# Kernel optimization log

Hardware: AMD Instinct MI355X
Metric: run time of the kernel (lower is better)

The kernel has to match this reference:

```python
import jax, jax.numpy as jnp
import numpy as np

HIDDEN_DIM = 1024
NUM_EXPERTS = 8
BASE_LR = 0.5
LR_DECAY = 0.85
TOLERANCE = 0.001


def setup_inputs() -> dict:
    key = jax.random.key(0)
    ks = jax.random.split(key, 8)
    B, T, D, E = 4, 2048, HIDDEN_DIM, NUM_EXPERTS
    x_real = jax.random.normal(ks[0], (B, T, D), dtype=jnp.float32)
    x_imag = jax.random.normal(ks[1], (B, T, D), dtype=jnp.float32)
    phase_offset = jax.random.uniform(ks[2], (D,), dtype=jnp.float32) * 2.0 * np.pi
    Wg = jax.random.normal(ks[3], (D, E), dtype=jnp.float32) / np.sqrt(D)
    bg = jnp.zeros((E,), dtype=jnp.float32)
    We = jax.random.normal(ks[4], (E, D, D), dtype=jnp.float32) / np.sqrt(D)
    be = jnp.zeros((E, D), dtype=jnp.float32)
    return {"x_real": x_real, "x_imag": x_imag, "phase_offset": phase_offset,
            "Wg": Wg, "bg": bg, "We": We, "be": be, "local_iterations": 8}


def _moe(z, Wg, bg, We, be, capacity):
    # z: [N, D] complex64. Expert-choice routing on the real part.
    N, D = z.shape
    logits = z.real @ Wg + bg                     # [N, E]
    S = jax.nn.softmax(logits, axis=-1)           # [N, E]
    scores, idx = jax.lax.top_k(S.T, capacity)    # each [E, k]
    gathered = z[idx]                             # [E, k, D] complex
    out_e = jnp.einsum('ekd,edh->ekh', gathered, We.astype(z.dtype)) + be[:, None, :]
    y = jnp.zeros((N, D), z.dtype).at[idx.reshape(-1)].add(
        (scores[..., None] * out_e).reshape(-1, D))
    return y


def _build_target(z, phase_offset):
    # z: [B, T, D] complex; target[t] = z[t-1] * exp(i*phase), target[0] = z[0]
    rot = jnp.exp(1j * phase_offset)              # [D] complex64
    return jnp.concatenate([z[:, :1, :], z[:, :-1, :] * rot], axis=1)


def reference(x_real, x_imag, phase_offset, Wg, bg, We, be, local_iterations):
    B, T, D = x_real.shape
    N = B * T
    capacity = N // NUM_EXPERTS
    z0 = (x_real + 1j * x_imag).astype(jnp.complex64)  # [B, T, D]
    target = _build_target(z0, phase_offset)
    max_iters = max(1, int(local_iterations) - 1)

    def cond(carry):
        it, z, lr, done = carry
        return jnp.logical_and(it < max_iters, jnp.logical_not(done))

    def body(carry):
        it, z, lr, _ = carry
        pred = _moe(z.reshape(N, D), Wg, bg, We, be, capacity).reshape(B, T, D)
        residual = target - pred
        z = z + lr.astype(z.dtype) * residual
        res_mean = jnp.mean(jnp.abs(residual))
        return (it + 1, z, lr * LR_DECAY, res_mean < TOLERANCE)

    it0 = jnp.array(0, jnp.int32)
    lr0 = jnp.array(BASE_LR, jnp.float32)
    iters_run, z_final, _, _ = jax.lax.while_loop(cond, body, (it0, z0, lr0, jnp.array(False)))

    target_grad = _build_target(z0, phase_offset)
    pred_grad = _moe(z_final.reshape(N, D), Wg, bg, We, be, capacity).reshape(B, T, D)
    out = z_final + BASE_LR * (target_grad - pred_grad)   # [B, T, D] complex
    out_stacked = jnp.stack([out.real, out.imag], axis=-1)  # [B, T, D, 2] float32
    return out_stacked, iters_run
```

## Files before the change

kernel.cpp:

```cpp
#include <hip/hip_runtime.h>
#include <math.h>

#define ND    8388608
#define NTOK  8192
#define DIM   1024
#define NEXP  8
#define CAP   1024
#define TSEQ  2048

typedef short bf16x8 __attribute__((ext_vector_type(8)));
typedef unsigned short u16x8 __attribute__((ext_vector_type(8)));
typedef float f32x4 __attribute__((ext_vector_type(4)));

#define AS1 __attribute__((address_space(1)))
#define AS3 __attribute__((address_space(3)))

__device__ __forceinline__ void gload_lds16(const void* g, void* l) {
    __builtin_amdgcn_global_load_lds((const AS1 unsigned int*)g,
                                     (AS3 unsigned int*)l, 16, 0, 0);
}

__device__ __forceinline__ unsigned short f2bf(float x) {
    union { float f; unsigned u; } v; v.f = x;
    unsigned r = v.u + 0x7FFFu + ((v.u >> 16) & 1u);
    return (unsigned short)(r >> 16);
}
__device__ __forceinline__ float bf2f(unsigned short b) {
    union { unsigned u; float f; } v; v.u = ((unsigned)b) << 16; return v.f;
}

__global__ void k_init_small(const float* __restrict__ phase, const int* __restrict__ Lptr,
                             float* __restrict__ rc, float* __restrict__ rs,
                             int* __restrict__ ctl) {
    int d = blockIdx.x * blockDim.x + threadIdx.x;
    if (d < DIM) { rc[d] = cosf(phase[d]); rs[d] = sinf(phase[d]); }
    if (d == 0) {
        ctl[0] = 0; ctl[1] = 0;
        int L = Lptr[0]; int mi = L - 1; if (mi < 1) mi = 1;
        ctl[2] = mi;
    }
}

__global__ void k_init_big(const float* __restrict__ xr, const float* __restrict__ xi,
                           float* __restrict__ zre, unsigned short* __restrict__ zimB) {
    int i = blockIdx.x * blockDim.x + threadIdx.x;
    if (i >= ND) return;
    zre[i] = xr[i];
    zimB[i] = f2bf(xi[i]);
}

__global__ __launch_bounds__(256) void k_wconv(const float* __restrict__ We,
                                               unsigned short* __restrict__ Whi,
                                               unsigned short* __restrict__ Wlo) {
    __shared__ float lds[64][65];
    int e = blockIdx.z, h0 = blockIdx.x * 64, d0 = blockIdx.y * 64;
    int tid = threadIdx.x;
    #pragma unroll
    for (int q = 0; q < 16; ++q) {
        int idx = q * 256 + tid;
        int i = idx >> 6, j = idx & 63;
        lds[i][j] = We[(size_t)e * 1048576 + (size_t)(d0 + i) * 1024 + h0 + j];
    }
    __syncthreads();
    #pragma unroll
    for (int q = 0; q < 2; ++q) {
        int sid = q * 256 + tid;
        int j = sid >> 3, sp = sid & 7;
        int h = h0 + j;
        int slog = sp ^ (h & 7);
        u16x8 hi, lo;
        #pragma unroll
        for (int u = 0; u < 8; ++u) {
            float x = lds[slog * 8 + u][j];
            unsigned short hb = f2bf(x);
            hi[u] = hb;
            lo[u] = f2bf(x - bf2f(hb));
        }
        size_t o = (((size_t)(e << 10) + h) << 10) + d0 + sp * 8;
        *(u16x8*)(Whi + o) = hi;
        *(u16x8*)(Wlo + o) = lo;
    }
}

__global__ __launch_bounds__(256) void k_gate(
    const float* __restrict__ zre, const float* __restrict__ Wg, const float* __restrict__ bg,
    float* __restrict__ S, int* __restrict__ tokcnt,
    const int* __restrict__ ctl, int iter) {
    if (iter >= 0 && (ctl[0] || iter >= ctl[2])) return;
    const int w = threadIdx.x >> 6, lane = threadIdx.x & 63;
    const int n = blockIdx.x * 4 + w;
    const float* zr = zre + ((size_t)n << 10);
    float acc[8] = {0,0,0,0,0,0,0,0};
    #pragma unroll
    for (int q = 0; q < 4; ++q) {
        const int d0 = q * 256 + lane * 4;
        float4 zv = *(const float4*)(zr + d0);
        float zz[4] = {zv.x, zv.y, zv.z, zv.w};
        #pragma unroll
        for (int j = 0; j < 4; ++j) {
            const float4 w0 = *(const float4*)(Wg + (d0 + j) * 8);
            const float4 w1 = *(const float4*)(Wg + (d0 + j) * 8 + 4);
            acc[0] += zz[j] * w0.x; acc[1] += zz[j] * w0.y; acc[2] += zz[j] * w0.z; acc[3] += zz[j] * w0.w;
            acc[4] += zz[j] * w1.x; acc[5] += zz[j] * w1.y; acc[6] += zz[j] * w1.z; acc[7] += zz[j] * w1.w;
        }
    }
    #pragma unroll
    for (int off = 32; off > 0; off >>= 1)
        #pragma unroll
        for (int e = 0; e < 8; ++e) acc[e] += __shfl_xor(acc[e], off);
    if (lane == 0) {
        float m = -1e30f;
        #pragma unroll
        for (int e = 0; e < 8; ++e) { acc[e] += bg[e]; m = fmaxf(m, acc[e]); }
        float sum = 0.f;
        #pragma unroll
        for (int e = 0; e < 8; ++e) { acc[e] = expf(acc[e] - m); sum += acc[e]; }
        float inv = 1.0f / sum;
        *(float4*)(S + (n << 3))     = (float4){acc[0]*inv, acc[1]*inv, acc[2]*inv, acc[3]*inv};
        *(float4*)(S + (n << 3) + 4) = (float4){acc[4]*inv, acc[5]*inv, acc[6]*inv, acc[7]*inv};
        tokcnt[n] = 0;
    }
}

__global__ __launch_bounds__(1024) void k_route(
    const float* __restrict__ S, int* __restrict__ idxs, int* __restrict__ tokcnt,
    int* __restrict__ ent_id, const int* __restrict__ ctl, int iter) {
    if (iter >= 0 && (ctl[0] || iter >= ctl[2])) return;
    __shared__ unsigned keys[NTOK];
    __shared__ unsigned hA[2048];
    __shared__ unsigned hB[2048];
    __shared__ int sbkt, srem, sntie, scnt;
    const int e = blockIdx.x, tid = threadIdx.x;
    if (tid == 0) scnt = 0;
    for (int n = tid; n < NTOK; n += 1024) keys[n] = __float_as_uint(S[(n << 3) + e]);
    __syncthreads();

    int rem = CAP;
    unsigned pref = 0;
    #pragma unroll
    for (int lvl = 0; lvl < 3; ++lvl) {
        const int nb = (lvl == 2) ? 1024 : 2048;
        for (int i = tid; i < nb; i += 1024) hA[i] = 0;
        __syncthreads();
        for (int n = tid; n < NTOK; n += 1024) {
            unsigned k = keys[n];
            bool ok; unsigned b;
            if (lvl == 0)      { ok = true;                 b = k >> 21; }
            else if (lvl == 1) { ok = (k >> 21) == pref;    b = (k >> 10) & 2047u; }
            else               { ok = (k >> 10) == pref;    b = k & 1023u; }
            if (ok) atomicAdd(&hA[b], 1u);
        }
        __syncthreads();
        unsigned* src = hA; unsigned* dst = hB;
        for (int off = 1; off < nb; off <<= 1) {
            for (int i = tid; i < nb; i += 1024)
                dst[i] = src[i] + ((i + off < nb) ? src[i + off] : 0u);
            __syncthreads();
            unsigned* t = src; src = dst; dst = t;
        }
        for (int i = tid; i < nb; i += 1024) {
            unsigned sfi = src[i];
            unsigned sfn = (i + 1 < nb) ? src[i + 1] : 0u;
            if (sfi >= (unsigned)rem && sfn < (unsigned)rem) {
                sbkt = i; srem = rem - (int)sfn; sntie = (int)(sfi - sfn);
            }
        }
        __syncthreads();
        int b = sbkt; rem = srem;
        if (lvl == 0)      pref = (unsigned)b;
        else if (lvl == 1) pref = (pref << 11) | (unsigned)b;
        else               pref = (pref << 10) | (unsigned)b;
        __syncthreads();
    }
    const unsigned T = pref;
    const int remv = rem;
    const bool allt = (remv == sntie);

    for (int n = tid; n < NTOK; n += 1024) {
        unsigned k = keys[n];
        bool sel = (k > T);
        if (k == T) {
            if (allt) sel = true;
            else {
                int r = 0;
                int j = 0;
                for (; j + 8 <= n; j += 8) {
                    r += (int)(keys[j] == T) + (int)(keys[j+1] == T) + (int)(keys[j+2] == T)
                       + (int)(keys[j+3] == T) + (int)(keys[j+4] == T) + (int)(keys[j+5] == T)
                       + (int)(keys[j+6] == T) + (int)(keys[j+7] == T);
                }
                for (; j < n; ++j) r += (int)(keys[j] == T);
                sel = (r < remv);
            }
        }
        if (sel) {
            int slot = atomicAdd(&scnt, 1);
            int row = (e << 10) + slot;
            idxs[row] = n;
            int p = atomicAdd(&tokcnt[n], 1);
            ent_id[(n << 3) + p] = row;
        }
    }
}

__global__ __launch_bounds__(256) void k_gather_convert(
    const float* __restrict__ zre, const int* __restrict__ idxs,
    unsigned short* __restrict__ Ahi, unsigned short* __restrict__ Alo,
    const int* __restrict__ ctl, int iter) {
    if (iter >= 0 && (ctl[0] || iter >= ctl[2])) return;
    int g = blockIdx.x * 256 + threadIdx.x;
    int r = g >> 7;
    int sl = g & 127;
    int c = sl >> 3, sp = sl & 7;
    int slog = sp ^ (r & 7);
    int n = idxs[r];
    const float* src = zre + ((size_t)n << 10) + c * 64 + slog * 8;
    u16x8 hi, lo;
    #pragma unroll
    for (int u = 0; u < 8; ++u) {
        float x = src[u];
        unsigned short hb = f2bf(x);
        hi[u] = hb;
        lo[u] = f2bf(x - bf2f(hb));
    }
    size_t o = ((size_t)r << 10) + c * 64 + sp * 8;
    *(u16x8*)(Ahi + o) = hi;
    *(u16x8*)(Alo + o) = lo;
}

__global__ __launch_bounds__(256, 2) void k_gemm_cx(
    const unsigned short* __restrict__ Ahi, const unsigned short* __restrict__ Alo,
    const unsigned short* __restrict__ zimB,
    const unsigned short* __restrict__ Whi, const unsigned short* __restrict__ Wlo,
    const float* __restrict__ be, const int* __restrict__ idxs,
    float* __restrict__ outre, float* __restrict__ outim,
    const int* __restrict__ ctl, int iter) {
    if (iter >= 0 && (ctl[0] || iter >= ctl[2])) return;
    extern __shared__ unsigned short smem[];
    const int bid = blockIdx.x;
    const int e = bid & 7, bx = (bid >> 3) & 7, by = bid >> 6;
    const int tid = threadIdx.x;
    const int wid = tid >> 6, lane = tid & 63;
    const int wm = wid >> 1, wn = wid & 1;

    const unsigned short* srcbase;
    int rowbase, tofs;
    if (wid == 0)      { srcbase = Ahi; rowbase = (e << 10) + by * 128; tofs = 0; }
    else if (wid == 1) { srcbase = Alo; rowbase = (e << 10) + by * 128; tofs = 8192; }
    else if (wid == 2) { srcbase = Whi; rowbase = (e << 10) + bx * 128; tofs = 24576; }
    else               { srcbase = Wlo; rowbase = (e << 10) + bx * 128; tofs = 32768; }
    const unsigned short* gsrc = srcbase + (((size_t)(rowbase + (lane >> 3))) << 10) + ((lane & 7) << 3);
    unsigned short* ldst = smem + tofs;

    const int rl = lane >> 3;
    const int ch = lane & 7;
    const int swzst = (ch ^ rl) << 3;
    int tok[4];
    #pragma unroll
    for (int q = 0; q < 4; ++q)
        tok[q] = idxs[(e << 10) + by * 128 + (wid << 5) + (q << 3) + rl];

    f32x4 accre[4][4], accim[4][4];
    #pragma unroll
    for (int a = 0; a < 4; ++a)
        #pragma unroll
        for (int b = 0; b < 4; ++b) {
            accre[a][b] = (f32x4){0.f, 0.f, 0.f, 0.f};
            accim[a][b] = (f32x4){0.f, 0.f, 0.f, 0.f};
        }

    for (int kt = 0; kt < DIM; kt += 64) {
        if (kt) __syncthreads();
        #pragma unroll
        for (int i = 0; i < 16; ++i)
            gload_lds16(gsrc + kt + ((size_t)i << 13), ldst + i * 512);
        u16x8 tmp[4];
        #pragma unroll
        for (int q = 0; q < 4; ++q)
            tmp[q] = *(const u16x8*)(zimB + ((size_t)tok[q] << 10) + kt + swzst);
        #pragma unroll
        for (int q = 0; q < 4; ++q) {
            int r = (wid << 5) + (q << 3) + rl;
            *(u16x8*)&smem[16384 + (r << 6) + (ch << 3)] = tmp[q];
        }
        __syncthreads();
        #pragma unroll
        for (int ks = 0; ks < 2; ++ks) {
            const int slog = (ks << 2) + (lane >> 4);
            const int swz = (slog ^ (lane & 7)) << 3;
            bf16x8 ah[4], al[4], am[4], bh[4], bl[4];
            #pragma unroll
            for (int mi = 0; mi < 4; ++mi) {
                int off = ((wm * 64 + mi * 16 + (lane & 15)) << 6) + swz;
                ah[mi] = *(const bf16x8*)&smem[off];
                al[mi] = *(const bf16x8*)&smem[8192 + off];
                am[mi] = *(const bf16x8*)&smem[16384 + off];
            }
            #pragma unroll
            for (int ni = 0; ni < 4; ++ni) {
                int off = ((wn * 64 + ni * 16 + (lane & 15)) << 6) + swz;
                bh[ni] = *(const bf16x8*)&smem[24576 + off];
                bl[ni] = *(const bf16x8*)&smem[32768 + off];
            }
            #pragma unroll
            for (int mi = 0; mi < 4; ++mi)
                #pragma unroll
                for (int ni = 0; ni < 4; ++ni) {
                    accre[mi][ni] = __builtin_amdgcn_mfma_f32_16x16x32_bf16(ah[mi], bh[ni], accre[mi][ni], 0, 0, 0);
                    accre[mi][ni] = __builtin_amdgcn_mfma_f32_16x16x32_bf16(ah[mi], bl[ni], accre[mi][ni], 0, 0, 0);
                    accre[mi][ni] = __builtin_amdgcn_mfma_f32_16x16x32_bf16(al[mi], bh[ni], accre[mi][ni], 0, 0, 0);
                    accim[mi][ni] = __builtin_amdgcn_mfma_f32_16x16x32_bf16(am[mi], bh[ni], accim[mi][ni], 0, 0, 0);
                }
        }
    }
    const int colbase = bx * 128 + wn * 64 + (lane & 15);
    float bev[4];
    #pragma unroll
    for (int ni = 0; ni < 4; ++ni) bev[ni] = be[(e << 10) + colbase + ni * 16];
    const int rowloc = by * 128 + wm * 64 + ((lane >> 4) << 2);
    float* obr = outre + (((size_t)(e << 10) + rowloc) << 10) + colbase;
    float* obi = outim + (((size_t)(e << 10) + rowloc) << 10) + colbase;
    #pragma unroll
    for (int mi = 0; mi < 4; ++mi)
        #pragma unroll
        for (int rg = 0; rg < 4; ++rg) {
            size_t ro = (size_t)(mi * 16 + rg) << 10;
            #pragma unroll
            for (int ni = 0; ni < 4; ++ni) {
                obr[ro + ni * 16] = accre[mi][ni][rg] + bev[ni];
                obi[ro + ni * 16] = accim[mi][ni][rg];
            }
        }
}

__global__ __launch_bounds__(256) void k_resid_gate(
    float* __restrict__ zre, unsigned short* __restrict__ zimB,
    const float* __restrict__ xr, const float* __restrict__ xi,
    const float* __restrict__ rc, const float* __restrict__ rs,
    const float* __restrict__ outre, const float* __restrict__ outim,
    int* __restrict__ tokcnt, const int* __restrict__ ent_id,
    float* __restrict__ S, const float* __restrict__ Wg, const float* __restrict__ bg,
    float lr, float* __restrict__ partial, const int* __restrict__ ctl, int iter) {
    if (ctl[0] || iter >= ctl[2]) return;
    __shared__ float wred[4][8];
    const int n = blockIdx.x;
    const int tid = threadIdx.x;
    const int d0 = tid << 2;
    const int kc = tokcnt[n];
    const int4 e0 = *(const int4*)(ent_id + (n << 3));
    const int4 e1 = *(const int4*)(ent_id + (n << 3) + 4);
    const int rows[8] = {e0.x, e0.y, e0.z, e0.w, e1.x, e1.y, e1.z, e1.w};

    float pr[4] = {0,0,0,0}, pm[4] = {0,0,0,0};
    #pragma unroll
    for (int k = 0; k < 8; ++k) {
        if (k < kc) {
            const int row = rows[k];
            const float s = S[(n << 3) + (row >> 10)];
            const float4 vr = *(const float4*)(outre + ((size_t)row << 10) + d0);
            const float4 vi = *(const float4*)(outim + ((size_t)row << 10) + d0);
            pr[0] += s * vr.x; pr[1] += s * vr.y; pr[2] += s * vr.z; pr[3] += s * vr.w;
            pm[0] += s * vi.x; pm[1] += s * vi.y; pm[2] += s * vi.z; pm[3] += s * vi.w;
        }
    }
    const size_t base = ((size_t)n << 10) + d0;
    const int t = n & (TSEQ - 1);
    float tr[4], ti[4];
    if (t == 0) {
        float4 a = *(const float4*)(xr + base), b = *(const float4*)(xi + base);
        tr[0]=a.x; tr[1]=a.y; tr[2]=a.z; tr[3]=a.w;
        ti[0]=b.x; ti[1]=b.y; ti[2]=b.z; ti[3]=b.w;
    } else {
        float4 a = *(const float4*)(xr + base - DIM), b = *(const float4*)(xi + base - DIM);
        float4 c = *(const float4*)(rc + d0), s4 = *(const float4*)(rs + d0);
        tr[0]=a.x*c.x-b.x*s4.x; tr[1]=a.y*c.y-b.y*s4.y; tr[2]=a.z*c.z-b.z*s4.z; tr[3]=a.w*c.w-b.w*s4.w;
        ti[0]=a.x*s4.x+b.x*c.x; ti[1]=a.y*s4.y+b.y*c.y; ti[2]=a.z*s4.z+b.z*c.z; ti[3]=a.w*s4.w+b.w*c.w;
    }
    float4 zr4 = *(const float4*)(zre + base);
    ushort4 zi4 = *(const ushort4*)(zimB + base);
    float zrv[4] = {zr4.x, zr4.y, zr4.z, zr4.w};
    unsigned short ziv[4] = {zi4.x, zi4.y, zi4.z, zi4.w};
    float zn[4]; unsigned short zo[4];
    float lsum = 0.f;
    float lac[8] = {0,0,0,0,0,0,0,0};
    #pragma unroll
    for (int j = 0; j < 4; ++j) {
        float rr = tr[j] - pr[j];
        float ri = ti[j] - pm[j];
        zn[j] = zrv[j] + lr * rr;
        zo[j] = f2bf(bf2f(ziv[j]) + lr * ri);
        lsum += sqrtf(rr * rr + ri * ri);
        const float4 w0 = *(const float4*)(Wg + (d0 + j) * 8);
        const float4 w1 = *(const float4*)(Wg + (d0 + j) * 8 + 4);
        lac[0] += zn[j] * w0.x; lac[1] += zn[j] * w0.y; lac[2] += zn[j] * w0.z; lac[3] += zn[j] * w0.w;
        lac[4] += zn[j] * w1.x; lac[5] += zn[j] * w1.y; lac[6] += zn[j] * w1.z; lac[7] += zn[j] * w1.w;
    }
    *(float4*)(zre + base) = (float4){zn[0], zn[1], zn[2], zn[3]};
    *(ushort4*)(zimB + base) = (ushort4){zo[0], zo[1], zo[2], zo[3]};

    const int w = tid >> 6, lane = tid & 63;
    #pragma unroll
    for (int off = 32; off > 0; off >>= 1) {
        lsum += __shfl_xor(lsum, off);
        #pragma unroll
        for (int e = 0; e < 8; ++e) lac[e] += __shfl_xor(lac[e], off);
    }
    if (lane == 0) {
        #pragma unroll
        for (int e = 0; e < 8; ++e) wred[w][e] = lac[e];
        partial[(n << 2) + w] = lsum;
    }
    __syncthreads();
    if (tid == 0) {
        float lg[8];
        float m = -1e30f;
        #pragma unroll
        for (int e = 0; e < 8; ++e) {
            lg[e] = wred[0][e] + wred[1][e] + wred[2][e] + wred[3][e] + bg[e];
            m = fmaxf(m, lg[e]);
        }
        float sum = 0.f;
        #pragma unroll
        for (int e = 0; e < 8; ++e) { lg[e] = expf(lg[e] - m); sum += lg[e]; }
        float inv = 1.0f / sum;
        *(float4*)(S + (n << 3))     = (float4){lg[0]*inv, lg[1]*inv, lg[2]*inv, lg[3]*inv};
        *(float4*)(S + (n << 3) + 4) = (float4){lg[4]*inv, lg[5]*inv, lg[6]*inv, lg[7]*inv};
        tokcnt[n] = 0;
    }
}

__global__ __launch_bounds__(1024) void k_finalize(
    const float* __restrict__ partial, int* __restrict__ ctl, int iter) {
    if (ctl[0] || iter >= ctl[2]) return;
    __shared__ float red[16];
    float s = 0.f;
    for (int i = threadIdx.x; i < NTOK * 4; i += 1024) s += partial[i];
    #pragma unroll
    for (int off = 32; off > 0; off >>= 1) s += __shfl_xor(s, off);
    if ((threadIdx.x & 63) == 0) red[threadIdx.x >> 6] = s;
    __syncthreads();
    if (threadIdx.x == 0) {
        float tot = 0.f;
        #pragma unroll
        for (int w = 0; w < 16; ++w) tot += red[w];
        ctl[1] = iter + 1;
        if (tot * (1.0f / (float)ND) < 0.001f) ctl[0] = 1;
    }
}

__global__ __launch_bounds__(256) void k_final_zupd(
    float* __restrict__ zre, unsigned short* __restrict__ zimB,
    const float* __restrict__ xr, const float* __restrict__ xi,
    const float* __restrict__ rc, const float* __restrict__ rs,
    const float* __restrict__ outre, const float* __restrict__ outim,
    const int* __restrict__ tokcnt, const int* __restrict__ ent_id,
    const float* __restrict__ S) {
    const int n = blockIdx.x;
    const int tid = threadIdx.x;
    const int d0 = tid << 2;
    const int kc = tokcnt[n];
    const int4 e0 = *(const int4*)(ent_id + (n << 3));
    const int4 e1 = *(const int4*)(ent_id + (n << 3) + 4);
    const int rows[8] = {e0.x, e0.y, e0.z, e0.w, e1.x, e1.y, e1.z, e1.w};
    float pr[4] = {0,0,0,0}, pm[4] = {0,0,0,0};
    #pragma unroll
    for (int k = 0; k < 8; ++k) {
        if (k < kc) {
            const int row = rows[k];
            const float s = S[(n << 3) + (row >> 10)];
            const float4 vr = *(const float4*)(outre + ((size_t)row << 10) + d0);
            const float4 vi = *(const float4*)(outim + ((size_t)row << 10) + d0);
            pr[0] += s * vr.x; pr[1] += s * vr.y; pr[2] += s * vr.z; pr[3] += s * vr.w;
            pm[0] += s * vi.x; pm[1] += s * vi.y; pm[2] += s * vi.z; pm[3] += s * vi.w;
        }
    }
    const size_t base = ((size_t)n << 10) + d0;
    const int t = n & (TSEQ - 1);
    float tr[4], ti[4];
    if (t == 0) {
        float4 a = *(const float4*)(xr + base), b = *(const float4*)(xi + base);
        tr[0]=a.x; tr[1]=a.y; tr[2]=a.z; tr[3]=a.w;
        ti[0]=b.x; ti[1]=b.y; ti[2]=b.z; ti[3]=b.w;
    } else {
        float4 a = *(const float4*)(xr + base - DIM), b = *(const float4*)(xi + base - DIM);
        float4 c = *(const float4*)(rc + d0), s4 = *(const float4*)(rs + d0);
        tr[0]=a.x*c.x-b.x*s4.x; tr[1]=a.y*c.y-b.y*s4.y; tr[2]=a.z*c.z-b.z*s4.z; tr[3]=a.w*c.w-b.w*s4.w;
        ti[0]=a.x*s4.x+b.x*c.x; ti[1]=a.y*s4.y+b.y*c.y; ti[2]=a.z*s4.z+b.z*c.z; ti[3]=a.w*s4.w+b.w*c.w;
    }
    float4 zr4 = *(const float4*)(zre + base);
    ushort4 zi4 = *(const ushort4*)(zimB + base);
    float zrv[4] = {zr4.x, zr4.y, zr4.z, zr4.w};
    unsigned short ziv[4] = {zi4.x, zi4.y, zi4.z, zi4.w};
    float zn[4]; unsigned short zo[4];
    #pragma unroll
    for (int j = 0; j < 4; ++j) {
        zn[j] = zrv[j] + 0.5f * (tr[j] - pr[j]);
        zo[j] = f2bf(bf2f(ziv[j]) + 0.5f * (ti[j] - pm[j]));
    }
    *(float4*)(zre + base) = (float4){zn[0], zn[1], zn[2], zn[3]};
    *(ushort4*)(zimB + base) = (ushort4){zo[0], zo[1], zo[2], zo[3]};
}

__global__ void k_write_out(const float* __restrict__ zre, const unsigned short* __restrict__ zimB,
                            float* __restrict__ out, const int* __restrict__ ctl) {
    int i = blockIdx.x * blockDim.x + threadIdx.x;
    if (i >= ND) return;
    out[2 * i]     = zre[i];
    out[2 * i + 1] = bf2f(zimB[i]);
    if (i == 0) out[(size_t)2 * ND] = (float)ctl[1];
}

extern "C" void kernel_launch(void* const* d_in, const int* in_sizes, int n_in,
                              void* d_out, int out_size, void* d_ws, size_t ws_size,
                              hipStream_t stream) {
    (void)in_sizes; (void)n_in; (void)out_size; (void)ws_size;
    const float* x_real = (const float*)d_in[0];
    const float* x_imag = (const float*)d_in[1];
    const float* phase  = (const float*)d_in[2];
    const float* Wg     = (const float*)d_in[3];
    const float* bg     = (const float*)d_in[4];
    const float* We     = (const float*)d_in[5];
    const float* be     = (const float*)d_in[6];
    const int*   Lptr   = (const int*)d_in[7];

    char* wsb = (char*)d_ws;
    float*          zre  = (float*)wsb;
    unsigned short* zimB = (unsigned short*)(wsb + 33554432);
    unsigned short* Ahi  = (unsigned short*)(wsb + 50331648);
    unsigned short* Alo  = (unsigned short*)(wsb + 67108864);
    unsigned short* Whi  = (unsigned short*)(wsb + 83886080);
    unsigned short* Wlo  = (unsigned short*)(wsb + 100663296);
    float*    S       = (float*)(wsb + 117440512);
    int*      ent_id  = (int*)  (wsb + 117702656);
    int*      idxs    = (int*)  (wsb + 117964800);
    int*      tokcnt  = (int*)  (wsb + 117997568);
    float*    partial = (float*)(wsb + 118030336);
    float*    rc      = (float*)(wsb + 118161408);
    float*    rs      = (float*)(wsb + 118165504);
    int*      ctl     = (int*)  (wsb + 118169600);

    float* outre = (float*)d_out;
    float* outim = outre + (size_t)ND;

    k_init_small<<<4, 256, 0, stream>>>(phase, Lptr, rc, rs, ctl);
    k_init_big<<<ND / 256, 256, 0, stream>>>(x_real, x_imag, zre, zimB);
    k_wconv<<<dim3(16, 16, 8), 256, 0, stream>>>(We, Whi, Wlo);
    k_gate<<<NTOK / 4, 256, 0, stream>>>(zre, Wg, bg, S, tokcnt, ctl, -1);

    const size_t gemm_lds = 40960 * sizeof(unsigned short);
    float lr = 0.5f;
    for (int it = 0; it < 7; ++it) {
        k_route<<<NEXP, 1024, 0, stream>>>(S, idxs, tokcnt, ent_id, ctl, it);
        k_gather_convert<<<4096, 256, 0, stream>>>(zre, idxs, Ahi, Alo, ctl, it);
        k_gemm_cx<<<512, 256, gemm_lds, stream>>>(Ahi, Alo, zimB, Whi, Wlo, be, idxs,
                                                  outre, outim, ctl, it);
        k_resid_gate<<<NTOK, 256, 0, stream>>>(zre, zimB, x_real, x_imag, rc, rs,
                                               outre, outim, tokcnt, ent_id, S, Wg, bg,
                                               lr, partial, ctl, it);
        k_finalize<<<1, 1024, 0, stream>>>(partial, ctl, it);
        lr *= 0.85f;
    }

    k_route<<<NEXP, 1024, 0, stream>>>(S, idxs, tokcnt, ent_id, ctl, -1);
    k_gather_convert<<<4096, 256, 0, stream>>>(zre, idxs, Ahi, Alo, ctl, -1);
    k_gemm_cx<<<512, 256, gemm_lds, stream>>>(Ahi, Alo, zimB, Whi, Wlo, be, idxs,
                                              outre, outim, ctl, -1);
    k_final_zupd<<<NTOK, 256, 0, stream>>>(zre, zimB, x_real, x_imag, rc, rs,
                                           outre, outim, tokcnt, ent_id, S);
    k_write_out<<<ND / 256, 256, 0, stream>>>(zre, zimB, (float*)d_out, ctl);
}
```

Before: 1.281 ms.

## Fuse gather and bf16 hi/lo split of z.real into the expert GEMM

Removes the separate gather_convert kernel, which wrote split bf16 hi/lo copies of the gathered real activations to global memory. The GEMM instead loads fp32 rows of z.real by token index, splits them into hi/lo bf16 in registers, and writes them straight to LDS. This saves a kernel launch and a 32MB write plus re-read each iteration. In exchange, every bx tile block repeats the gather and conversion (8x redundant fp32 reads), and the A loads become synchronous register loads instead of async global-to-LDS.

```diff
diff --git a/kernel.cpp b/kernel.cpp
--- a/kernel.cpp
+++ b/kernel.cpp
@@ -203,34 +203,8 @@
     }
 }
 
-__global__ __launch_bounds__(256) void k_gather_convert(
-    const float* __restrict__ zre, const int* __restrict__ idxs,
-    unsigned short* __restrict__ Ahi, unsigned short* __restrict__ Alo,
-    const int* __restrict__ ctl, int iter) {
-    if (iter >= 0 && (ctl[0] || iter >= ctl[2])) return;
-    int g = blockIdx.x * 256 + threadIdx.x;
-    int r = g >> 7;
-    int sl = g & 127;
-    int c = sl >> 3, sp = sl & 7;
-    int slog = sp ^ (r & 7);
-    int n = idxs[r];
-    const float* src = zre + ((size_t)n << 10) + c * 64 + slog * 8;
-    u16x8 hi, lo;
-    #pragma unroll
-    for (int u = 0; u < 8; ++u) {
-        float x = src[u];
-        unsigned short hb = f2bf(x);
-        hi[u] = hb;
-        lo[u] = f2bf(x - bf2f(hb));
-    }
-    size_t o = ((size_t)r << 10) + c * 64 + sp * 8;
-    *(u16x8*)(Ahi + o) = hi;
-    *(u16x8*)(Alo + o) = lo;
-}
-
 __global__ __launch_bounds__(256, 2) void k_gemm_cx(
-    const unsigned short* __restrict__ Ahi, const unsigned short* __restrict__ Alo,
-    const unsigned short* __restrict__ zimB,
+    const float* __restrict__ zre, const unsigned short* __restrict__ zimB,
     const unsigned short* __restrict__ Whi, const unsigned short* __restrict__ Wlo,
     const float* __restrict__ be, const int* __restrict__ idxs,
     float* __restrict__ outre, float* __restrict__ outim,
@@ -243,18 +217,18 @@
     const int wid = tid >> 6, lane = tid & 63;
     const int wm = wid >> 1, wn = wid & 1;
 
-    const unsigned short* srcbase;
-    int rowbase, tofs;
-    if (wid == 0)      { srcbase = Ahi; rowbase = (e << 10) + by * 128; tofs = 0; }
-    else if (wid == 1) { srcbase = Alo; rowbase = (e << 10) + by * 128; tofs = 8192; }
-    else if (wid == 2) { srcbase = Whi; rowbase = (e << 10) + bx * 128; tofs = 24576; }
-    else               { srcbase = Wlo; rowbase = (e << 10) + bx * 128; tofs = 32768; }
-    const unsigned short* gsrc = srcbase + (((size_t)(rowbase + (lane >> 3))) << 10) + ((lane & 7) << 3);
-    unsigned short* ldst = smem + tofs;
+    const unsigned short* gsrc = nullptr;
+    unsigned short* ldst = nullptr;
+    if (wid >= 2) {
+        const unsigned short* wsb = (wid == 2) ? Whi : Wlo;
+        int rowbase = (e << 10) + bx * 128;
+        gsrc = wsb + (((size_t)(rowbase + (lane >> 3))) << 10) + ((lane & 7) << 3);
+        ldst = smem + ((wid == 2) ? 24576 : 32768);
+    }
 
     const int rl = lane >> 3;
     const int ch = lane & 7;
-    const int swzst = (ch ^ rl) << 3;
+    const int slog8 = (ch ^ rl) << 3;
     int tok[4];
     #pragma unroll
     for (int q = 0; q < 4; ++q)
@@ -271,17 +245,35 @@
 
     for (int kt = 0; kt < DIM; kt += 64) {
         if (kt) __syncthreads();
-        #pragma unroll
-        for (int i = 0; i < 16; ++i)
-            gload_lds16(gsrc + kt + ((size_t)i << 13), ldst + i * 512);
-        u16x8 tmp[4];
-        #pragma unroll
-        for (int q = 0; q < 4; ++q)
-            tmp[q] = *(const u16x8*)(zimB + ((size_t)tok[q] << 10) + kt + swzst);
+        if (wid >= 2) {
+            #pragma unroll
+            for (int i = 0; i < 16; ++i)
+                gload_lds16(gsrc + kt + ((size_t)i << 13), ldst + i * 512);
+        }
+        float4 a0[4], a1[4]; u16x8 im[4];
         #pragma unroll
         for (int q = 0; q < 4; ++q) {
-            int r = (wid << 5) + (q << 3) + rl;
-            *(u16x8*)&smem[16384 + (r << 6) + (ch << 3)] = tmp[q];
+            const float* zsrc = zre + ((size_t)tok[q] << 10) + kt + slog8;
+            a0[q] = *(const float4*)zsrc;
+            a1[q] = *(const float4*)(zsrc + 4);
+            im[q] = *(const u16x8*)(zimB + ((size_t)tok[q] << 10) + kt + slog8);
+        }
+        #pragma unroll
+        for (int q = 0; q < 4; ++q) {
+            const int r = (wid << 5) + (q << 3) + rl;
+            const int lo_off = (r << 6) + (ch << 3);
+            float xv[8] = {a0[q].x, a0[q].y, a0[q].z, a0[q].w,
+                           a1[q].x, a1[q].y, a1[q].z, a1[q].w};
+            u16x8 hi, lo;
+            #pragma unroll
+            for (int u = 0; u < 8; ++u) {
+                unsigned short hb = f2bf(xv[u]);
+                hi[u] = hb;
+                lo[u] = f2bf(xv[u] - bf2f(hb));
+            }
+            *(u16x8*)&smem[lo_off]         = hi;
+            *(u16x8*)&smem[8192 + lo_off]  = lo;
+            *(u16x8*)&smem[16384 + lo_off] = im[q];
         }
         __syncthreads();
         #pragma unroll
@@ -526,18 +518,16 @@
     char* wsb = (char*)d_ws;
     float*          zre  = (float*)wsb;
     unsigned short* zimB = (unsigned short*)(wsb + 33554432);
-    unsigned short* Ahi  = (unsigned short*)(wsb + 50331648);
-    unsigned short* Alo  = (unsigned short*)(wsb + 67108864);
-    unsigned short* Whi  = (unsigned short*)(wsb + 83886080);
-    unsigned short* Wlo  = (unsigned short*)(wsb + 100663296);
-    float*    S       = (float*)(wsb + 117440512);
-    int*      ent_id  = (int*)  (wsb + 117702656);
-    int*      idxs    = (int*)  (wsb + 117964800);
-    int*      tokcnt  = (int*)  (wsb + 117997568);
-    float*    partial = (float*)(wsb + 118030336);
-    float*    rc      = (float*)(wsb + 118161408);
-    float*    rs      = (float*)(wsb + 118165504);
-    int*      ctl     = (int*)  (wsb + 118169600);
+    unsigned short* Whi  = (unsigned short*)(wsb + 50331648);
+    unsigned short* Wlo  = (unsigned short*)(wsb + 67108864);
+    float*    S       = (float*)(wsb + 83886080);
+    int*      ent_id  = (int*)  (wsb + 84148224);
+    int*      idxs    = (int*)  (wsb + 84410368);
+    int*      tokcnt  = (int*)  (wsb + 84443136);
+    float*    partial = (float*)(wsb + 84475904);
+    float*    rc      = (float*)(wsb + 84606976);
+    float*    rs      = (float*)(wsb + 84611072);
+    int*      ctl     = (int*)  (wsb + 84615168);
 
     float* outre = (float*)d_out;
     float* outim = outre + (size_t)ND;
@@ -551,8 +541,7 @@
     float lr = 0.5f;
     for (int it = 0; it < 7; ++it) {
         k_route<<<NEXP, 1024, 0, stream>>>(S, idxs, tokcnt, ent_id, ctl, it);
-        k_gather_convert<<<4096, 256, 0, stream>>>(zre, idxs, Ahi, Alo, ctl, it);
-        k_gemm_cx<<<512, 256, gemm_lds, stream>>>(Ahi, Alo, zimB, Whi, Wlo, be, idxs,
+        k_gemm_cx<<<512, 256, gemm_lds, stream>>>(zre, zimB, Whi, Wlo, be, idxs,
                                                   outre, outim, ctl, it);
         k_resid_gate<<<NTOK, 256, 0, stream>>>(zre, zimB, x_real, x_imag, rc, rs,
                                                outre, outim, tokcnt, ent_id, S, Wg, bg,
@@ -562,8 +551,7 @@
     }
 
     k_route<<<NEXP, 1024, 0, stream>>>(S, idxs, tokcnt, ent_id, ctl, -1);
-    k_gather_convert<<<4096, 256, 0, stream>>>(zre, idxs, Ahi, Alo, ctl, -1);
-    k_gemm_cx<<<512, 256, gemm_lds, stream>>>(Ahi, Alo, zimB, Whi, Wlo, be, idxs,
+    k_gemm_cx<<<512, 256, gemm_lds, stream>>>(zre, zimB, Whi, Wlo, be, idxs,
                                               outre, outim, ctl, -1);
     k_final_zupd<<<NTOK, 256, 0, stream>>>(zre, zimB, x_real, x_imag, rc, rs,
                                            outre, outim, tokcnt, ent_id, S);
```

Result: faster. 1.239 ms (-3.3%).
